# Kernel tuning notes

Hardware: AMD Instinct MI355X
Metric: run time of the kernel (lower is better)

The kernel has to match this reference:

```python
import jax, jax.numpy as jnp
import numpy as np

B, E, H, F, L, A = 256, 1024, 1024, 2048, 196, 512
C_RATIO, H_RATIO = 0.5, 0.5


def setup_inputs() -> dict:
    key = jax.random.key(0)
    ks = jax.random.split(key, 20)
    u = lambda k, shape: jax.random.uniform(k, shape, jnp.float32, -0.1, 0.1)
    return {
        "xt": jax.random.normal(ks[0], (B, E), jnp.float32),
        "att_seq": jax.random.normal(ks[1], (B, L, F), jnp.float32),
        "h": jax.random.normal(ks[2], (B, H), jnp.float32),
        "c": jax.random.normal(ks[3], (B, H), jnp.float32),
        "Wi": u(ks[4], (4 * H, E)), "bi": u(ks[5], (4 * H,)),
        "Wh": u(ks[6], (4 * H, H)), "bh": u(ks[7], (4 * H,)),
        "Wz": u(ks[8], (4 * H, F)), "bz": u(ks[9], (4 * H,)),
        "Wa": u(ks[10], (A, F)), "ba": u(ks[11], (A,)),
        "Wha": u(ks[12], (A, H)), "bha": u(ks[13], (A,)),
        "Wo": u(ks[14], (1, A)), "bo": u(ks[15], (1,)),
    }


def reference(xt, att_seq, h, c, Wi, bi, Wh, bh, Wz, bz, Wa, ba, Wha, bha, Wo, bo):
    # attention scoring: tanh(att_2_att_h(att) + h_2_att_h(h)) -> scalar per location
    att_linear = jnp.einsum("blf,af->bla", att_seq, Wa) + ba          # [B,L,A]
    h_linear = h @ Wha.T + bha                                        # [B,A]
    att_h = jnp.tanh(att_linear + h_linear[:, None, :])               # [B,L,A]
    scores = jnp.einsum("bla,a->bl", att_h, Wo[0]) + bo[0]            # [B,L]
    w = jax.nn.softmax(scores, axis=-1)                               # [B,L]
    z = jnp.einsum("bl,blf->bf", w, att_seq)                          # [B,F] context

    # fused LSTM gates
    sums = (xt @ Wi.T + bi) + (h @ Wh.T + bh) + (z @ Wz.T + bz)       # [B,4H]
    i_g = jax.nn.sigmoid(sums[:, 0 * H:1 * H])
    f_g = jax.nn.sigmoid(sums[:, 1 * H:2 * H])
    o_g = jax.nn.sigmoid(sums[:, 2 * H:3 * H])
    g = jnp.tanh(sums[:, 3 * H:4 * H])

    # zoneout blending (training mode; dropout prob is 0 -> identity)
    next_c = c * C_RATIO + (1.0 - C_RATIO) * (f_g * c + i_g * g)
    next_h = h * H_RATIO + (1.0 - H_RATIO) * (o_g * jnp.tanh(next_c))
    return next_h, next_h, next_c  # (output, state_h, state_c)
```

## Files before the change

### kernel.cpp

```cpp
#include <hip/hip_runtime.h>

#define B_ 256
#define E_ 1024
#define H_ 1024
#define F_ 2048
#define L_ 196
#define A_ 512
#define ML (B_ * L_)

typedef __attribute__((ext_vector_type(8))) short short8;
typedef __attribute__((ext_vector_type(4))) float f32x4;

__device__ __forceinline__ unsigned short f2bf(float x) {
  unsigned u = __float_as_uint(x);
  unsigned r = (u + 0x7FFFu + ((u >> 16) & 1u)) >> 16;
  return (unsigned short)r;
}
__device__ __forceinline__ float bf2f(unsigned short u) {
  return __uint_as_float((unsigned)u << 16);
}
__device__ __forceinline__ float fast_tanh(float x) {
  x = fminf(fmaxf(x, -15.f), 15.f);
  float e = __expf(2.f * x);
  return (e - 1.f) / (e + 1.f);
}
__device__ __forceinline__ float sigmoidf_(float x) {
  return 1.f / (1.f + __expf(-x));
}

#define GLOAD_LDS(gptr, lptr) \
  __builtin_amdgcn_global_load_lds( \
      (const __attribute__((address_space(1))) void*)(gptr), \
      (__attribute__((address_space(3))) void*)(lptr), 16, 0, 0)

#define SBAR() asm volatile("s_barrier" ::: "memory")

__global__ void cast_att_k(const float* __restrict__ src, unsigned short* __restrict__ dst) {
  size_t i = ((size_t)blockIdx.x * 256 + threadIdx.x) * 8;
  float4 a = *reinterpret_cast<const float4*>(src + i);
  float4 b = *reinterpret_cast<const float4*>(src + i + 4);
  short8 o;
  o[0] = (short)f2bf(a.x); o[1] = (short)f2bf(a.y); o[2] = (short)f2bf(a.z); o[3] = (short)f2bf(a.w);
  o[4] = (short)f2bf(b.x); o[5] = (short)f2bf(b.y); o[6] = (short)f2bf(b.z); o[7] = (short)f2bf(b.w);
  *reinterpret_cast<short8*>(dst + i) = o;
}

__global__ void cast_w_all_k(const float* __restrict__ Wa, const float* __restrict__ Wha,
                             const float* __restrict__ Wi, const float* __restrict__ Wh,
                             const float* __restrict__ Wz,
                             unsigned short* __restrict__ WaB, unsigned short* __restrict__ WhaB,
                             unsigned short* __restrict__ WgB) {
  size_t i = ((size_t)blockIdx.x * 256 + threadIdx.x) * 8;
  const float* src;
  unsigned short* dst;
  if (i < 1048576) { src = Wa + i; dst = WaB + i; }
  else if (i < 1572864) { src = Wha + (i - 1048576); dst = WhaB + (i - 1048576); }
  else {
    size_t off = i - 1572864;
    int row = (int)(off >> 12), col = (int)(off & 4095);
    if (col < 1024)       src = Wi + (size_t)row * 1024 + col;
    else if (col < 2048)  src = Wh + (size_t)row * 1024 + (col - 1024);
    else                  src = Wz + (size_t)row * 2048 + (col - 2048);
    dst = WgB + off;
  }
  float4 a = *reinterpret_cast<const float4*>(src);
  float4 b = *reinterpret_cast<const float4*>(src + 4);
  short8 o;
  o[0] = (short)f2bf(a.x); o[1] = (short)f2bf(a.y); o[2] = (short)f2bf(a.z); o[3] = (short)f2bf(a.w);
  o[4] = (short)f2bf(b.x); o[5] = (short)f2bf(b.y); o[6] = (short)f2bf(b.z); o[7] = (short)f2bf(b.w);
  *reinterpret_cast<short8*>(dst) = o;
}

__global__ void cast_xh_k(const float* __restrict__ xt, const float* __restrict__ h,
                          unsigned short* __restrict__ AgB) {
  int i = (blockIdx.x * 256 + threadIdx.x) * 8;
  int row = i >> 11;
  int col = i & 2047;
  const float* src = (col < 1024) ? (xt + row * 1024 + col) : (h + row * 1024 + (col - 1024));
  float4 a = *reinterpret_cast<const float4*>(src);
  float4 b = *reinterpret_cast<const float4*>(src + 4);
  short8 o;
  o[0] = (short)f2bf(a.x); o[1] = (short)f2bf(a.y); o[2] = (short)f2bf(a.z); o[3] = (short)f2bf(a.w);
  o[4] = (short)f2bf(b.x); o[5] = (short)f2bf(b.y); o[6] = (short)f2bf(b.z); o[7] = (short)f2bf(b.w);
  *reinterpret_cast<short8*>(AgB + (size_t)row * 4096 + col) = o;
}

__global__ __launch_bounds__(256, 2)
void hlin_gemm_k(const unsigned short* __restrict__ AgB, const unsigned short* __restrict__ WhaB,
                 const float* __restrict__ bha, float* __restrict__ hlin) {
  __shared__ unsigned short As[2][64 * 64];
  __shared__ unsigned short Bs[2][128 * 64];
  const int tid = threadIdx.x;
  const int lane = tid & 63, wid = tid >> 6;
  const int wm = wid >> 1, wn = wid & 1;
  const int m0 = blockIdx.y * 64;
  const int n0 = blockIdx.x * 128;
  const int g16 = lane >> 4, l16 = lane & 15;
  const int l7 = l16 & 7;
  f32x4 acc[2][4] = {};

#define STAGE_HL(BUF, KK)                                                                      \
  {                                                                                            \
    _Pragma("unroll")                                                                          \
    for (int it = 0; it < 2; ++it) {                                                           \
      int idx = it * 256 + tid;                                                                \
      int row = idx >> 3;                                                                      \
      int kc = (idx & 7) ^ (row & 7);                                                          \
      GLOAD_LDS(AgB + (size_t)(m0 + row) * 4096 + 1024 + (KK) + kc * 8, &As[BUF][idx * 8]);    \
    }                                                                                          \
    _Pragma("unroll")                                                                          \
    for (int it = 0; it < 4; ++it) {                                                           \
      int idx = it * 256 + tid;                                                                \
      int row = idx >> 3;                                                                      \
      int kc = (idx & 7) ^ (row & 7);                                                          \
      GLOAD_LDS(WhaB + (size_t)(n0 + row) * 1024 + (KK) + kc * 8, &Bs[BUF][idx * 8]);          \
    }                                                                                          \
  }

  STAGE_HL(0, 0);
  STAGE_HL(1, 64);
  asm volatile("s_waitcnt vmcnt(6)" ::: "memory");
  SBAR();
  int cur = 0;
  for (int k0 = 0; k0 < 1024; k0 += 64) {
    #pragma unroll
    for (int ks = 0; ks < 2; ++ks) {
      const int ko = ((ks * 4 + g16) ^ l7) << 3;
      short8 af[2], bfr[4];
      #pragma unroll
      for (int mi = 0; mi < 2; ++mi)
        af[mi] = *reinterpret_cast<const short8*>(&As[cur][(wm * 32 + mi * 16 + l16) * 64 + ko]);
      #pragma unroll
      for (int ni = 0; ni < 4; ++ni)
        bfr[ni] = *reinterpret_cast<const short8*>(&Bs[cur][(wn * 64 + ni * 16 + l16) * 64 + ko]);
      #pragma unroll
      for (int mi = 0; mi < 2; ++mi)
        #pragma unroll
        for (int ni = 0; ni < 4; ++ni)
          acc[mi][ni] = __builtin_amdgcn_mfma_f32_16x16x32_bf16(af[mi], bfr[ni], acc[mi][ni], 0, 0, 0);
    }
    SBAR();
    if (k0 + 128 < 1024) {
      STAGE_HL(cur, k0 + 128);
      asm volatile("s_waitcnt vmcnt(6)" ::: "memory");
    } else {
      asm volatile("s_waitcnt vmcnt(0)" ::: "memory");
    }
    SBAR();
    cur ^= 1;
  }
#undef STAGE_HL

  #pragma unroll
  for (int ni = 0; ni < 4; ++ni) {
    int col = n0 + wn * 64 + ni * 16 + l16;
    float bv = bha[col];
    #pragma unroll
    for (int mi = 0; mi < 2; ++mi)
      #pragma unroll
      for (int j = 0; j < 4; ++j) {
        int m = m0 + wm * 32 + mi * 16 + g16 * 4 + j;
        hlin[(size_t)m * A_ + col] = acc[mi][ni][j] + bv;
      }
  }
}

__global__ __launch_bounds__(256, 2)
void score_pre_k(const unsigned short* __restrict__ attB, const unsigned short* __restrict__ WaB,
                 const float* __restrict__ hlin, const float* __restrict__ ba,
                 const float* __restrict__ Wo, float* __restrict__ scores8) {
  __shared__ unsigned short As[2][128 * 64];
  __shared__ unsigned short Bs[2][128 * 64];
  const int tid = threadIdx.x;
  const int lane = tid & 63, wid = tid >> 6;
  const int wm = wid >> 1, wn = wid & 1;
  const int logical = (blockIdx.x & 7) * 196 + (blockIdx.x >> 3);
  const int m0 = (logical >> 2) * 128;
  const int n0 = (logical & 3) * 128;
  const int g16 = lane >> 4, l16 = lane & 15;
  const int l7 = l16 & 7;
  f32x4 acc[4][4] = {};

#define STAGE_SC(BUF, KK)                                                                \
  {                                                                                      \
    _Pragma("unroll")                                                                    \
    for (int it = 0; it < 4; ++it) {                                                     \
      int idx = it * 256 + tid;                                                          \
      int row = idx >> 3;                                                                \
      int kc = (idx & 7) ^ (row & 7);                                                    \
      GLOAD_LDS(WaB + (size_t)(n0 + row) * F_ + (KK) + kc * 8, &Bs[BUF][idx * 8]);       \
      GLOAD_LDS(attB + (size_t)(m0 + row) * F_ + (KK) + kc * 8, &As[BUF][idx * 8]);      \
    }                                                                                    \
  }

  STAGE_SC(0, 0);
  STAGE_SC(1, 64);
  asm volatile("s_waitcnt vmcnt(8)" ::: "memory");
  SBAR();
  int cur = 0;
  for (int k0 = 0; k0 < F_; k0 += 64) {
    #pragma unroll
    for (int ks = 0; ks < 2; ++ks) {
      const int ko = ((ks * 4 + g16) ^ l7) << 3;
      short8 af[4], bfr[4];
      #pragma unroll
      for (int mi = 0; mi < 4; ++mi)
        af[mi] = *reinterpret_cast<const short8*>(&As[cur][(wm * 64 + mi * 16 + l16) * 64 + ko]);
      #pragma unroll
      for (int ni = 0; ni < 4; ++ni)
        bfr[ni] = *reinterpret_cast<const short8*>(&Bs[cur][(wn * 64 + ni * 16 + l16) * 64 + ko]);
      #pragma unroll
      for (int mi = 0; mi < 4; ++mi)
        #pragma unroll
        for (int ni = 0; ni < 4; ++ni)
          acc[mi][ni] = __builtin_amdgcn_mfma_f32_16x16x32_bf16(af[mi], bfr[ni], acc[mi][ni], 0, 0, 0);
    }
    SBAR();
    if (k0 + 128 < F_) {
      STAGE_SC(cur, k0 + 128);
      asm volatile("s_waitcnt vmcnt(8)" ::: "memory");
    } else {
      asm volatile("s_waitcnt vmcnt(0)" ::: "memory");
    }
    SBAR();
    cur ^= 1;
  }
#undef STAGE_SC

  float wo_v[4], ba_v[4];
  int a_v[4];
  #pragma unroll
  for (int ni = 0; ni < 4; ++ni) {
    int a = n0 + wn * 64 + ni * 16 + l16;
    a_v[ni] = a; wo_v[ni] = Wo[a]; ba_v[ni] = ba[a];
  }
  const int slot = (n0 >> 7) * 2 + wn;
  #pragma unroll
  for (int mi = 0; mi < 4; ++mi) {
    float rs[4];
    #pragma unroll
    for (int j = 0; j < 4; ++j) {
      int m = m0 + wm * 64 + mi * 16 + g16 * 4 + j;
      int b = m / L_;
      const float* hb = hlin + (size_t)b * A_;
      float s = 0.f;
      #pragma unroll
      for (int ni = 0; ni < 4; ++ni) {
        float v = acc[mi][ni][j] + ba_v[ni] + hb[a_v[ni]];
        s += fast_tanh(v) * wo_v[ni];
      }
      rs[j] = s;
    }
    #pragma unroll
    for (int off = 1; off < 16; off <<= 1) {
      #pragma unroll
      for (int j = 0; j < 4; ++j) rs[j] += __shfl_xor(rs[j], off);
    }
    if (l16 == 0) {
      #pragma unroll
      for (int j = 0; j < 4; ++j) {
        int m = m0 + wm * 64 + mi * 16 + g16 * 4 + j;
        scores8[(size_t)m * 8 + slot] = rs[j];
      }
    }
  }
}

__global__ __launch_bounds__(256, 2)
void score_fb_k(const float* __restrict__ att, const unsigned short* __restrict__ WaB,
                const float* __restrict__ hlin, const float* __restrict__ ba,
                const float* __restrict__ Wo, float* __restrict__ scores8) {
  __shared__ unsigned short As[2][128 * 64];
  __shared__ unsigned short Bs[2][128 * 64];
  const int tid = threadIdx.x;
  const int lane = tid & 63, wid = tid >> 6;
  const int wm = wid >> 1, wn = wid & 1;
  const int logical = (blockIdx.x & 7) * 196 + (blockIdx.x >> 3);
  const int m0 = (logical >> 2) * 128;
  const int n0 = (logical & 3) * 128;
  const int g16 = lane >> 4, l16 = lane & 15;
  const int l7 = l16 & 7;
  f32x4 acc[4][4] = {};

#define STAGE_FB(BUF, KK)                                                               \
  {                                                                                     \
    _Pragma("unroll")                                                                   \
    for (int it = 0; it < 4; ++it) {                                                    \
      int idx = it * 256 + tid;                                                         \
      int row = idx >> 3;                                                               \
      int kc = (idx & 7) ^ (row & 7);                                                   \
      GLOAD_LDS(WaB + (size_t)(n0 + row) * F_ + (KK) + kc * 8, &Bs[BUF][idx * 8]);      \
    }                                                                                   \
    _Pragma("unroll")                                                                   \
    for (int it = 0; it < 8; ++it) {                                                    \
      int idx = it * 256 + tid;                                                         \
      int row = idx >> 4, kf = idx & 15;                                                \
      float4 v = *reinterpret_cast<const float4*>(att + (size_t)(m0 + row) * F_ + (KK) + kf * 4); \
      ushort4 o;                                                                        \
      o.x = f2bf(v.x); o.y = f2bf(v.y); o.z = f2bf(v.z); o.w = f2bf(v.w);               \
      int el = row * 64 + (((kf >> 1) ^ (row & 7)) << 3) + ((kf & 1) << 2);             \
      *reinterpret_cast<ushort4*>(&As[BUF][el]) = o;                                    \
    }                                                                                   \
  }

  int cur = 0;
  STAGE_FB(0, 0);
  __syncthreads();
  for (int k0 = 0; k0 < F_; k0 += 64) {
    if (k0 + 64 < F_) STAGE_FB(cur ^ 1, k0 + 64);
    #pragma unroll
    for (int ks = 0; ks < 2; ++ks) {
      const int ko = ((ks * 4 + g16) ^ l7) << 3;
      short8 af[4], bfr[4];
      #pragma unroll
      for (int mi = 0; mi < 4; ++mi)
        af[mi] = *reinterpret_cast<const short8*>(&As[cur][(wm * 64 + mi * 16 + l16) * 64 + ko]);
      #pragma unroll
      for (int ni = 0; ni < 4; ++ni)
        bfr[ni] = *reinterpret_cast<const short8*>(&Bs[cur][(wn * 64 + ni * 16 + l16) * 64 + ko]);
      #pragma unroll
      for (int mi = 0; mi < 4; ++mi)
        #pragma unroll
        for (int ni = 0; ni < 4; ++ni)
          acc[mi][ni] = __builtin_amdgcn_mfma_f32_16x16x32_bf16(af[mi], bfr[ni], acc[mi][ni], 0, 0, 0);
    }
    __syncthreads();
    cur ^= 1;
  }
#undef STAGE_FB

  float wo_v[4], ba_v[4];
  int a_v[4];
  #pragma unroll
  for (int ni = 0; ni < 4; ++ni) {
    int a = n0 + wn * 64 + ni * 16 + l16;
    a_v[ni] = a; wo_v[ni] = Wo[a]; ba_v[ni] = ba[a];
  }
  const int slot = (n0 >> 7) * 2 + wn;
  #pragma unroll
  for (int mi = 0; mi < 4; ++mi) {
    float rs[4];
    #pragma unroll
    for (int j = 0; j < 4; ++j) {
      int m = m0 + wm * 64 + mi * 16 + g16 * 4 + j;
      int b = m / L_;
      const float* hb = hlin + (size_t)b * A_;
      float s = 0.f;
      #pragma unroll
      for (int ni = 0; ni < 4; ++ni) {
        float v = acc[mi][ni][j] + ba_v[ni] + hb[a_v[ni]];
        s += fast_tanh(v) * wo_v[ni];
      }
      rs[j] = s;
    }
    #pragma unroll
    for (int off = 1; off < 16; off <<= 1) {
      #pragma unroll
      for (int j = 0; j < 4; ++j) rs[j] += __shfl_xor(rs[j], off);
    }
    if (l16 == 0) {
      #pragma unroll
      for (int j = 0; j < 4; ++j) {
        int m = m0 + wm * 64 + mi * 16 + g16 * 4 + j;
        scores8[(size_t)m * 8 + slot] = rs[j];
      }
    }
  }
}

__global__ __launch_bounds__(256)
void z_sm_k(const unsigned short* __restrict__ attB, const float* __restrict__ scores8,
            unsigned short* __restrict__ AgB) {
  __shared__ float sm[L_];
  const int b = blockIdx.y;
  const int tid = threadIdx.x;
  if (tid < L_) {
    const float* p = scores8 + ((size_t)b * L_ + tid) * 8;
    float4 p0 = *reinterpret_cast<const float4*>(p);
    float4 p1 = *reinterpret_cast<const float4*>(p + 4);
    sm[tid] = (p0.x + p0.y) + (p0.z + p0.w) + (p1.x + p1.y) + (p1.z + p1.w);
  }
  __syncthreads();
  float mx = -1e30f;
  for (int l = 0; l < L_; ++l) mx = fmaxf(mx, sm[l]);
  float s = 0.f;
  for (int l = 0; l < L_; ++l) s += __expf(sm[l] - mx);
  const float inv = 1.f / s;
  __syncthreads();
  if (tid < L_) sm[tid] = __expf(sm[tid] - mx) * inv;
  __syncthreads();
  const int f0 = blockIdx.x * 1024 + tid * 4;
  const unsigned short* base = attB + (size_t)b * L_ * F_ + f0;
  float a0 = 0.f, a1 = 0.f, a2 = 0.f, a3 = 0.f;
  #pragma unroll 4
  for (int l = 0; l < L_; ++l) {
    float wl = sm[l];
    ushort4 a = *reinterpret_cast<const ushort4*>(base + (size_t)l * F_);
    a0 += wl * bf2f(a.x); a1 += wl * bf2f(a.y); a2 += wl * bf2f(a.z); a3 += wl * bf2f(a.w);
  }
  ushort4 o;
  o.x = f2bf(a0); o.y = f2bf(a1); o.z = f2bf(a2); o.w = f2bf(a3);
  *reinterpret_cast<ushort4*>(AgB + (size_t)b * 4096 + 2048 + f0) = o;
}

__global__ __launch_bounds__(256)
void z_sm_f32_k(const float* __restrict__ att, const float* __restrict__ scores8,
                unsigned short* __restrict__ AgB) {
  __shared__ float sm[L_];
  const int b = blockIdx.y;
  const int tid = threadIdx.x;
  if (tid < L_) {
    const float* p = scores8 + ((size_t)b * L_ + tid) * 8;
    float4 p0 = *reinterpret_cast<const float4*>(p);
    float4 p1 = *reinterpret_cast<const float4*>(p + 4);
    sm[tid] = (p0.x + p0.y) + (p0.z + p0.w) + (p1.x + p1.y) + (p1.z + p1.w);
  }
  __syncthreads();
  float mx = -1e30f;
  for (int l = 0; l < L_; ++l) mx = fmaxf(mx, sm[l]);
  float s = 0.f;
  for (int l = 0; l < L_; ++l) s += __expf(sm[l] - mx);
  const float inv = 1.f / s;
  __syncthreads();
  if (tid < L_) sm[tid] = __expf(sm[tid] - mx) * inv;
  __syncthreads();
  const int f0 = blockIdx.x * 1024 + tid * 4;
  const float* base = att + (size_t)b * L_ * F_ + f0;
  float a0 = 0.f, a1 = 0.f, a2 = 0.f, a3 = 0.f;
  #pragma unroll 4
  for (int l = 0; l < L_; ++l) {
    float wl = sm[l];
    float4 a = *reinterpret_cast<const float4*>(base + (size_t)l * F_);
    a0 += wl * a.x; a1 += wl * a.y; a2 += wl * a.z; a3 += wl * a.w;
  }
  ushort4 o;
  o.x = f2bf(a0); o.y = f2bf(a1); o.z = f2bf(a2); o.w = f2bf(a3);
  *reinterpret_cast<ushort4*>(AgB + (size_t)b * 4096 + 2048 + f0) = o;
}

__global__ __launch_bounds__(256, 4)
void gates_gemm_k(const unsigned short* __restrict__ AgB, const unsigned short* __restrict__ WgB,
                  const float* __restrict__ bi, const float* __restrict__ bh,
                  const float* __restrict__ bz, float* __restrict__ sums) {
  __shared__ unsigned short As[2][64 * 64];
  __shared__ unsigned short Bs[2][64 * 64];
  const int tid = threadIdx.x;
  const int lane = tid & 63, wid = tid >> 6;
  const int wm = wid >> 1, wn = wid & 1;
  const int m0 = blockIdx.y * 64;
  const int n0 = blockIdx.x * 64;
  const int g16 = lane >> 4, l16 = lane & 15;
  const int l7 = l16 & 7;
  f32x4 acc[2][2] = {};

#define STAGE_GG(BUF, KK)                                                               \
  {                                                                                     \
    _Pragma("unroll")                                                                   \
    for (int it = 0; it < 2; ++it) {                                                    \
      int idx = it * 256 + tid;                                                         \
      int row = idx >> 3;                                                               \
      int kc = (idx & 7) ^ (row & 7);                                                   \
      GLOAD_LDS(AgB + (size_t)(m0 + row) * 4096 + (KK) + kc * 8, &As[BUF][idx * 8]);    \
      GLOAD_LDS(WgB + (size_t)(n0 + row) * 4096 + (KK) + kc * 8, &Bs[BUF][idx * 8]);    \
    }                                                                                   \
  }

  STAGE_GG(0, 0);
  STAGE_GG(1, 64);
  asm volatile("s_waitcnt vmcnt(4)" ::: "memory");
  SBAR();
  int cur = 0;
  for (int k0 = 0; k0 < 4096; k0 += 64) {
    #pragma unroll
    for (int ks = 0; ks < 2; ++ks) {
      const int ko = ((ks * 4 + g16) ^ l7) << 3;
      short8 af[2], bfr[2];
      #pragma unroll
      for (int mi = 0; mi < 2; ++mi)
        af[mi] = *reinterpret_cast<const short8*>(&As[cur][(wm * 32 + mi * 16 + l16) * 64 + ko]);
      #pragma unroll
      for (int ni = 0; ni < 2; ++ni)
        bfr[ni] = *reinterpret_cast<const short8*>(&Bs[cur][(wn * 32 + ni * 16 + l16) * 64 + ko]);
      #pragma unroll
      for (int mi = 0; mi < 2; ++mi)
        #pragma unroll
        for (int ni = 0; ni < 2; ++ni)
          acc[mi][ni] = __builtin_amdgcn_mfma_f32_16x16x32_bf16(af[mi], bfr[ni], acc[mi][ni], 0, 0, 0);
    }
    SBAR();
    if (k0 + 128 < 4096) {
      STAGE_GG(cur, k0 + 128);
      asm volatile("s_waitcnt vmcnt(4)" ::: "memory");
    } else {
      asm volatile("s_waitcnt vmcnt(0)" ::: "memory");
    }
    SBAR();
    cur ^= 1;
  }
#undef STAGE_GG

  #pragma unroll
  for (int ni = 0; ni < 2; ++ni) {
    int col = n0 + wn * 32 + ni * 16 + l16;
    float bsum = bi[col] + bh[col] + bz[col];
    #pragma unroll
    for (int mi = 0; mi < 2; ++mi)
      #pragma unroll
      for (int j = 0; j < 4; ++j) {
        int m = m0 + wm * 32 + mi * 16 + g16 * 4 + j;
        sums[(size_t)m * 4096 + col] = acc[mi][ni][j] + bsum;
      }
  }
}

__global__ void final_k(const float* __restrict__ sums, const float* __restrict__ h,
                        const float* __restrict__ c, float* __restrict__ out) {
  int i = blockIdx.x * 256 + threadIdx.x;
  int b = i >> 10, hh = i & 1023;
  const float* srow = sums + (size_t)b * 4096;
  float ig = sigmoidf_(srow[hh]);
  float fg = sigmoidf_(srow[1024 + hh]);
  float og = sigmoidf_(srow[2048 + hh]);
  float g  = fast_tanh(srow[3072 + hh]);
  float cv = c[i], hv = h[i];
  float nc = 0.5f * cv + 0.5f * (fg * cv + ig * g);
  float nh = 0.5f * hv + 0.5f * (og * fast_tanh(nc));
  out[i] = nh;
  out[B_ * H_ + i] = nh;
  out[2 * B_ * H_ + i] = nc;
}

extern "C" void kernel_launch(void* const* d_in, const int* in_sizes, int n_in,
                              void* d_out, int out_size, void* d_ws, size_t ws_size,
                              hipStream_t stream) {
  const float* xt  = (const float*)d_in[0];
  const float* att = (const float*)d_in[1];
  const float* h   = (const float*)d_in[2];
  const float* c   = (const float*)d_in[3];
  const float* Wi  = (const float*)d_in[4];
  const float* bi  = (const float*)d_in[5];
  const float* Wh  = (const float*)d_in[6];
  const float* bh  = (const float*)d_in[7];
  const float* Wz  = (const float*)d_in[8];
  const float* bz  = (const float*)d_in[9];
  const float* Wa  = (const float*)d_in[10];
  const float* ba  = (const float*)d_in[11];
  const float* Wha = (const float*)d_in[12];
  const float* bha = (const float*)d_in[13];
  const float* Wo  = (const float*)d_in[14];

  char* ws = (char*)d_ws;
  const size_t MB = (size_t)1 << 20;
  unsigned short* WaB  = (unsigned short*)(ws);
  unsigned short* WhaB = (unsigned short*)(ws + 2 * MB);
  unsigned short* WgB  = (unsigned short*)(ws + 3 * MB);
  unsigned short* AgB  = (unsigned short*)(ws + 35 * MB);
  float* hlin    = (float*)(ws + 37 * MB);
  float* scores8 = (float*)(ws + 38 * MB);
  float* sums    = (float*)(ws + 40 * MB);
  unsigned short* attB = (unsigned short*)(ws + 48 * MB);
  const bool PRE = ws_size >= 245 * MB;
  float* out = (float*)d_out;

  cast_w_all_k<<<8960, 256, 0, stream>>>(Wa, Wha, Wi, Wh, Wz, WaB, WhaB, WgB);
  cast_xh_k<<<256, 256, 0, stream>>>(xt, h, AgB);
  hlin_gemm_k<<<dim3(4, 4), 256, 0, stream>>>(AgB, WhaB, bha, hlin);
  if (PRE) {
    cast_att_k<<<ML, 256, 0, stream>>>(att, attB);
    score_pre_k<<<(ML / 128) * (A_ / 128), 256, 0, stream>>>(attB, WaB, hlin, ba, Wo, scores8);
    z_sm_k<<<dim3(2, B_), 256, 0, stream>>>(attB, scores8, AgB);
  } else {
    score_fb_k<<<(ML / 128) * (A_ / 128), 256, 0, stream>>>(att, WaB, hlin, ba, Wo, scores8);
    z_sm_f32_k<<<dim3(2, B_), 256, 0, stream>>>(att, scores8, AgB);
  }
  gates_gemm_k<<<dim3(64, 4), 256, 0, stream>>>(AgB, WgB, bi, bh, bz, sums);
  final_k<<<B_ * H_ / 256, 256, 0, stream>>>(sums, h, c, out);
}
```

Baseline: 421.4 us.

## Fuse att bf16 cast into score GEMM with register-staged prefetch

```diff
diff --git a/kernel.cpp b/kernel.cpp
--- a/kernel.cpp
+++ b/kernel.cpp
@@ -35,33 +35,29 @@
 
 #define SBAR() asm volatile("s_barrier" ::: "memory")
 
-__global__ void cast_att_k(const float* __restrict__ src, unsigned short* __restrict__ dst) {
-  size_t i = ((size_t)blockIdx.x * 256 + threadIdx.x) * 8;
-  float4 a = *reinterpret_cast<const float4*>(src + i);
-  float4 b = *reinterpret_cast<const float4*>(src + i + 4);
-  short8 o;
-  o[0] = (short)f2bf(a.x); o[1] = (short)f2bf(a.y); o[2] = (short)f2bf(a.z); o[3] = (short)f2bf(a.w);
-  o[4] = (short)f2bf(b.x); o[5] = (short)f2bf(b.y); o[6] = (short)f2bf(b.z); o[7] = (short)f2bf(b.w);
-  *reinterpret_cast<short8*>(dst + i) = o;
-}
-
-__global__ void cast_w_all_k(const float* __restrict__ Wa, const float* __restrict__ Wha,
-                             const float* __restrict__ Wi, const float* __restrict__ Wh,
-                             const float* __restrict__ Wz,
-                             unsigned short* __restrict__ WaB, unsigned short* __restrict__ WhaB,
-                             unsigned short* __restrict__ WgB) {
+__global__ void cast_wx_k(const float* __restrict__ Wa, const float* __restrict__ Wha,
+                          const float* __restrict__ Wi, const float* __restrict__ Wh,
+                          const float* __restrict__ Wz, const float* __restrict__ xt,
+                          const float* __restrict__ h,
+                          unsigned short* __restrict__ WaB, unsigned short* __restrict__ WhaB,
+                          unsigned short* __restrict__ WgB, unsigned short* __restrict__ AgB) {
   size_t i = ((size_t)blockIdx.x * 256 + threadIdx.x) * 8;
   const float* src;
   unsigned short* dst;
   if (i < 1048576) { src = Wa + i; dst = WaB + i; }
   else if (i < 1572864) { src = Wha + (i - 1048576); dst = WhaB + (i - 1048576); }
-  else {
+  else if (i < 18350080) {
     size_t off = i - 1572864;
     int row = (int)(off >> 12), col = (int)(off & 4095);
     if (col < 1024)       src = Wi + (size_t)row * 1024 + col;
     else if (col < 2048)  src = Wh + (size_t)row * 1024 + (col - 1024);
     else                  src = Wz + (size_t)row * 2048 + (col - 2048);
     dst = WgB + off;
+  } else {
+    size_t off = i - 18350080;
+    int row = (int)(off >> 11), col = (int)(off & 2047);
+    src = (col < 1024) ? (xt + (size_t)row * 1024 + col) : (h + (size_t)row * 1024 + (col - 1024));
+    dst = AgB + (size_t)row * 4096 + col;
   }
   float4 a = *reinterpret_cast<const float4*>(src);
   float4 b = *reinterpret_cast<const float4*>(src + 4);
@@ -69,20 +65,6 @@
   o[0] = (short)f2bf(a.x); o[1] = (short)f2bf(a.y); o[2] = (short)f2bf(a.z); o[3] = (short)f2bf(a.w);
   o[4] = (short)f2bf(b.x); o[5] = (short)f2bf(b.y); o[6] = (short)f2bf(b.z); o[7] = (short)f2bf(b.w);
   *reinterpret_cast<short8*>(dst) = o;
-}
-
-__global__ void cast_xh_k(const float* __restrict__ xt, const float* __restrict__ h,
-                          unsigned short* __restrict__ AgB) {
-  int i = (blockIdx.x * 256 + threadIdx.x) * 8;
-  int row = i >> 11;
-  int col = i & 2047;
-  const float* src = (col < 1024) ? (xt + row * 1024 + col) : (h + row * 1024 + (col - 1024));
-  float4 a = *reinterpret_cast<const float4*>(src);
-  float4 b = *reinterpret_cast<const float4*>(src + 4);
-  short8 o;
-  o[0] = (short)f2bf(a.x); o[1] = (short)f2bf(a.y); o[2] = (short)f2bf(a.z); o[3] = (short)f2bf(a.w);
-  o[4] = (short)f2bf(b.x); o[5] = (short)f2bf(b.y); o[6] = (short)f2bf(b.z); o[7] = (short)f2bf(b.w);
-  *reinterpret_cast<short8*>(AgB + (size_t)row * 4096 + col) = o;
 }
 
 __global__ __launch_bounds__(256, 2)
@@ -165,10 +147,12 @@
   }
 }
 
+template <bool WB>
 __global__ __launch_bounds__(256, 2)
-void score_pre_k(const unsigned short* __restrict__ attB, const unsigned short* __restrict__ WaB,
-                 const float* __restrict__ hlin, const float* __restrict__ ba,
-                 const float* __restrict__ Wo, float* __restrict__ scores8) {
+void score_fuse_k(const float* __restrict__ att, unsigned short* __restrict__ attB,
+                  const unsigned short* __restrict__ WaB,
+                  const float* __restrict__ hlin, const float* __restrict__ ba,
+                  const float* __restrict__ Wo, float* __restrict__ scores8) {
   __shared__ unsigned short As[2][128 * 64];
   __shared__ unsigned short Bs[2][128 * 64];
   const int tid = threadIdx.x;
@@ -180,8 +164,18 @@
   const int g16 = lane >> 4, l16 = lane & 15;
   const int l7 = l16 & 7;
   f32x4 acc[4][4] = {};
-
-#define STAGE_SC(BUF, KK)                                                                \
+  float4 a_reg[8];
+
+#define LOADA(KK)                                                                        \
+  {                                                                                      \
+    _Pragma("unroll")                                                                    \
+    for (int it = 0; it < 8; ++it) {                                                     \
+      int idx = it * 256 + tid;                                                          \
+      int row = idx >> 4, kf = idx & 15;                                                 \
+      a_reg[it] = *reinterpret_cast<const float4*>(att + (size_t)(m0 + row) * F_ + (KK) + kf * 4); \
+    }                                                                                    \
+  }
+#define GLDB(BUF, KK)                                                                    \
   {                                                                                      \
     _Pragma("unroll")                                                                    \
     for (int it = 0; it < 4; ++it) {                                                     \
@@ -189,14 +183,33 @@
       int row = idx >> 3;                                                                \
       int kc = (idx & 7) ^ (row & 7);                                                    \
       GLOAD_LDS(WaB + (size_t)(n0 + row) * F_ + (KK) + kc * 8, &Bs[BUF][idx * 8]);       \
-      GLOAD_LDS(attB + (size_t)(m0 + row) * F_ + (KK) + kc * 8, &As[BUF][idx * 8]);      \
     }                                                                                    \
   }
-
-  STAGE_SC(0, 0);
-  STAGE_SC(1, 64);
-  asm volatile("s_waitcnt vmcnt(8)" ::: "memory");
+#define WRITEA(BUF, KK)                                                                  \
+  {                                                                                      \
+    _Pragma("unroll")                                                                    \
+    for (int it = 0; it < 8; ++it) {                                                     \
+      int idx = it * 256 + tid;                                                          \
+      int row = idx >> 4, kf = idx & 15;                                                 \
+      float4 v = a_reg[it];                                                              \
+      ushort4 o;                                                                         \
+      o.x = f2bf(v.x); o.y = f2bf(v.y); o.z = f2bf(v.z); o.w = f2bf(v.w);                \
+      int el = row * 64 + (((kf >> 1) ^ (row & 7)) << 3) + ((kf & 1) << 2);              \
+      *reinterpret_cast<ushort4*>(&As[BUF][el]) = o;                                     \
+      if (WB && n0 == 0)                                                                 \
+        *reinterpret_cast<ushort4*>(attB + (size_t)(m0 + row) * F_ + (KK) + kf * 4) = o; \
+    }                                                                                    \
+  }
+
+  LOADA(0);
+  GLDB(0, 0);
+  asm volatile("s_waitcnt vmcnt(0)" ::: "memory");
+  WRITEA(0, 0);
+  LOADA(64);
+  GLDB(1, 64);
+  asm volatile("s_waitcnt lgkmcnt(0)" ::: "memory");
   SBAR();
+
   int cur = 0;
   for (int k0 = 0; k0 < F_; k0 += 64) {
     #pragma unroll
@@ -216,118 +229,21 @@
           acc[mi][ni] = __builtin_amdgcn_mfma_f32_16x16x32_bf16(af[mi], bfr[ni], acc[mi][ni], 0, 0, 0);
     }
     SBAR();
-    if (k0 + 128 < F_) {
-      STAGE_SC(cur, k0 + 128);
-      asm volatile("s_waitcnt vmcnt(8)" ::: "memory");
-    } else {
+    if (k0 + 64 < F_) {
       asm volatile("s_waitcnt vmcnt(0)" ::: "memory");
+      WRITEA(cur ^ 1, k0 + 64);
+      if (k0 + 128 < F_) {
+        LOADA(k0 + 128);
+        GLDB(cur, k0 + 128);
+      }
+      asm volatile("s_waitcnt lgkmcnt(0)" ::: "memory");
     }
     SBAR();
     cur ^= 1;
   }
-#undef STAGE_SC
-
-  float wo_v[4], ba_v[4];
-  int a_v[4];
-  #pragma unroll
-  for (int ni = 0; ni < 4; ++ni) {
-    int a = n0 + wn * 64 + ni * 16 + l16;
-    a_v[ni] = a; wo_v[ni] = Wo[a]; ba_v[ni] = ba[a];
-  }
-  const int slot = (n0 >> 7) * 2 + wn;
-  #pragma unroll
-  for (int mi = 0; mi < 4; ++mi) {
-    float rs[4];
-    #pragma unroll
-    for (int j = 0; j < 4; ++j) {
-      int m = m0 + wm * 64 + mi * 16 + g16 * 4 + j;
-      int b = m / L_;
-      const float* hb = hlin + (size_t)b * A_;
-      float s = 0.f;
-      #pragma unroll
-      for (int ni = 0; ni < 4; ++ni) {
-        float v = acc[mi][ni][j] + ba_v[ni] + hb[a_v[ni]];
-        s += fast_tanh(v) * wo_v[ni];
-      }
-      rs[j] = s;
-    }
-    #pragma unroll
-    for (int off = 1; off < 16; off <<= 1) {
-      #pragma unroll
-      for (int j = 0; j < 4; ++j) rs[j] += __shfl_xor(rs[j], off);
-    }
-    if (l16 == 0) {
-      #pragma unroll
-      for (int j = 0; j < 4; ++j) {
-        int m = m0 + wm * 64 + mi * 16 + g16 * 4 + j;
-        scores8[(size_t)m * 8 + slot] = rs[j];
-      }
-    }
-  }
-}
-
-__global__ __launch_bounds__(256, 2)
-void score_fb_k(const float* __restrict__ att, const unsigned short* __restrict__ WaB,
-                const float* __restrict__ hlin, const float* __restrict__ ba,
-                const float* __restrict__ Wo, float* __restrict__ scores8) {
-  __shared__ unsigned short As[2][128 * 64];
-  __shared__ unsigned short Bs[2][128 * 64];
-  const int tid = threadIdx.x;
-  const int lane = tid & 63, wid = tid >> 6;
-  const int wm = wid >> 1, wn = wid & 1;
-  const int logical = (blockIdx.x & 7) * 196 + (blockIdx.x >> 3);
-  const int m0 = (logical >> 2) * 128;
-  const int n0 = (logical & 3) * 128;
-  const int g16 = lane >> 4, l16 = lane & 15;
-  const int l7 = l16 & 7;
-  f32x4 acc[4][4] = {};
-
-#define STAGE_FB(BUF, KK)                                                               \
-  {                                                                                     \
-    _Pragma("unroll")                                                                   \
-    for (int it = 0; it < 4; ++it) {                                                    \
-      int idx = it * 256 + tid;                                                         \
-      int row = idx >> 3;                                                               \
-      int kc = (idx & 7) ^ (row & 7);                                                   \
-      GLOAD_LDS(WaB + (size_t)(n0 + row) * F_ + (KK) + kc * 8, &Bs[BUF][idx * 8]);      \
-    }                                                                                   \
-    _Pragma("unroll")                                                                   \
-    for (int it = 0; it < 8; ++it) {                                                    \
-      int idx = it * 256 + tid;                                                         \
-      int row = idx >> 4, kf = idx & 15;                                                \
-      float4 v = *reinterpret_cast<const float4*>(att + (size_t)(m0 + row) * F_ + (KK) + kf * 4); \
-      ushort4 o;                                                                        \
-      o.x = f2bf(v.x); o.y = f2bf(v.y); o.z = f2bf(v.z); o.w = f2bf(v.w);               \
-      int el = row * 64 + (((kf >> 1) ^ (row & 7)) << 3) + ((kf & 1) << 2);             \
-      *reinterpret_cast<ushort4*>(&As[BUF][el]) = o;                                    \
-    }                                                                                   \
-  }
-
-  int cur = 0;
-  STAGE_FB(0, 0);
-  __syncthreads();
-  for (int k0 = 0; k0 < F_; k0 += 64) {
-    if (k0 + 64 < F_) STAGE_FB(cur ^ 1, k0 + 64);
-    #pragma unroll
-    for (int ks = 0; ks < 2; ++ks) {
-      const int ko = ((ks * 4 + g16) ^ l7) << 3;
-      short8 af[4], bfr[4];
-      #pragma unroll
-      for (int mi = 0; mi < 4; ++mi)
-        af[mi] = *reinterpret_cast<const short8*>(&As[cur][(wm * 64 + mi * 16 + l16) * 64 + ko]);
-      #pragma unroll
-      for (int ni = 0; ni < 4; ++ni)
-        bfr[ni] = *reinterpret_cast<const short8*>(&Bs[cur][(wn * 64 + ni * 16 + l16) * 64 + ko]);
-      #pragma unroll
-      for (int mi = 0; mi < 4; ++mi)
-        #pragma unroll
-        for (int ni = 0; ni < 4; ++ni)
-          acc[mi][ni] = __builtin_amdgcn_mfma_f32_16x16x32_bf16(af[mi], bfr[ni], acc[mi][ni], 0, 0, 0);
-    }
-    __syncthreads();
-    cur ^= 1;
-  }
-#undef STAGE_FB
+#undef LOADA
+#undef GLDB
+#undef WRITEA
 
   float wo_v[4], ba_v[4];
   int a_v[4];
@@ -559,18 +475,16 @@
   float* scores8 = (float*)(ws + 38 * MB);
   float* sums    = (float*)(ws + 40 * MB);
   unsigned short* attB = (unsigned short*)(ws + 48 * MB);
-  const bool PRE = ws_size >= 245 * MB;
+  const bool BIG = ws_size >= 245 * MB;
   float* out = (float*)d_out;
 
-  cast_w_all_k<<<8960, 256, 0, stream>>>(Wa, Wha, Wi, Wh, Wz, WaB, WhaB, WgB);
-  cast_xh_k<<<256, 256, 0, stream>>>(xt, h, AgB);
+  cast_wx_k<<<9216, 256, 0, stream>>>(Wa, Wha, Wi, Wh, Wz, xt, h, WaB, WhaB, WgB, AgB);
   hlin_gemm_k<<<dim3(4, 4), 256, 0, stream>>>(AgB, WhaB, bha, hlin);
-  if (PRE) {
-    cast_att_k<<<ML, 256, 0, stream>>>(att, attB);
-    score_pre_k<<<(ML / 128) * (A_ / 128), 256, 0, stream>>>(attB, WaB, hlin, ba, Wo, scores8);
+  if (BIG) {
+    score_fuse_k<true><<<(ML / 128) * (A_ / 128), 256, 0, stream>>>(att, attB, WaB, hlin, ba, Wo, scores8);
     z_sm_k<<<dim3(2, B_), 256, 0, stream>>>(attB, scores8, AgB);
   } else {
-    score_fb_k<<<(ML / 128) * (A_ / 128), 256, 0, stream>>>(att, WaB, hlin, ba, Wo, scores8);
+    score_fuse_k<false><<<(ML / 128) * (A_ / 128), 256, 0, stream>>>(att, attB, WaB, hlin, ba, Wo, scores8);
     z_sm_f32_k<<<dim3(2, B_), 256, 0, stream>>>(att, scores8, AgB);
   }
   gates_gemm_k<<<dim3(64, 4), 256, 0, stream>>>(AgB, WgB, bi, bh, bz, sums);
```

Result: no change. 418.2 us (-0.8%).
